# Kernel tuning notes

Measured on AMD Instinct MI355X. Metric: run time of the kernel, lower is better.

Reference implementation:

```python
import jax, jax.numpy as jnp
import numpy as np

N_NODES = 20000
N_EDGES = 160000
IN_DIM = 2048
HID = 512


def setup_inputs() -> dict:
    key = jax.random.key(0)
    ks = jax.random.split(key, 12)
    s1 = 1.0 / np.sqrt(IN_DIM)
    s2 = 1.0 / np.sqrt(HID)
    return {
        "x": jax.random.normal(ks[0], (N_NODES, IN_DIM), dtype=jnp.float32),
        "edge_index": jax.random.randint(ks[1], (2, N_EDGES), 0, N_NODES, dtype=jnp.int64),
        "W1": jax.random.uniform(ks[2], (IN_DIM, HID), jnp.float32, -s1, s1),
        "b1": jax.random.uniform(ks[3], (HID,), jnp.float32, -s1, s1),
        "W2": jax.random.uniform(ks[4], (HID, HID), jnp.float32, -s2, s2),
        "b2": jax.random.uniform(ks[5], (HID,), jnp.float32, -s2, s2),
        "Wg": jax.random.uniform(ks[6], (HID, HID), jnp.float32, -s2, s2),
        "bg": jax.random.uniform(ks[7], (HID,), jnp.float32, -s2, s2),
        "Wa": jax.random.uniform(ks[8], (HID, 1), jnp.float32, -s2, s2),
        "ba": jax.random.uniform(ks[9], (1,), jnp.float32, -s2, s2),
    }


def reference(x, edge_index, W1, b1, W2, b2, Wg, bg, Wa, ba):
    # GINConv (eps=0): h = MLP((1+eps)*x + sum_{j in N(i)} x_j)
    src, dst = edge_index[0], edge_index[1]
    agg = jax.ops.segment_sum(x[src], dst, num_segments=x.shape[0])  # [N, IN_DIM]
    h = x + agg
    h = jnp.maximum(h @ W1 + b1, 0.0) @ W2 + b2  # [N, HID]
    # Gated attention pooling scores
    A = jnp.tanh(h @ Wg + bg)                    # [N, HID]
    alpha = (A @ Wa + ba)[:, 0]                  # [N]
    att_scores = jax.nn.softmax(alpha, axis=0)   # softmax over all nodes
    return (h, att_scores)
```

## Files before the change

### kernel.cpp

```cpp
#include <hip/hip_runtime.h>

typedef __attribute__((ext_vector_type(8))) __bf16 bf16x8;
typedef __attribute__((ext_vector_type(4))) __bf16 bf16x4;
typedef __attribute__((ext_vector_type(4))) float f32x4;
typedef __attribute__((ext_vector_type(8))) unsigned short u16x8;

__device__ __forceinline__ bf16x8 cvt8(float4 a, float4 b) {
    bf16x8 o;
    o[0] = (__bf16)a.x; o[1] = (__bf16)a.y; o[2] = (__bf16)a.z; o[3] = (__bf16)a.w;
    o[4] = (__bf16)b.x; o[5] = (__bf16)b.y; o[6] = (__bf16)b.z; o[7] = (__bf16)b.w;
    return o;
}
__device__ __forceinline__ bf16x4 cvt4(f32x4 v) {
    bf16x4 o;
    o[0] = (__bf16)v[0]; o[1] = (__bf16)v[1]; o[2] = (__bf16)v[2]; o[3] = (__bf16)v[3];
    return o;
}

__device__ __forceinline__ unsigned swz(int row, int s) {
    return (unsigned)((row * 64 + s * 16) ^ ((row & 8) << 2));
}

#define GLDS(g, l) __builtin_amdgcn_global_load_lds(                        \
    (const __attribute__((address_space(1))) void*)(g),                     \
    (__attribute__((address_space(3))) void*)(l), 16, 0, 0)

__global__ __launch_bounds__(256) void convw_pre_kernel(const float* __restrict__ W,
                                                        char* __restrict__ out, int K) {
    int t = blockIdx.x * 256 + threadIdx.x;
    if (t >= K * 512) return;
    int k = t >> 9, n = t & 511;
    int cb = n >> 8, r = n & 255, tt = k >> 5, s = (k & 31) >> 3, e = k & 7;
    size_t off = ((size_t)cb * (K >> 5) + tt) * 16384 + swz(r, s) + e * 2;
    *(__bf16*)(out + off) = (__bf16)W[t];
}

__global__ __launch_bounds__(256) void count_kernel(const int* __restrict__ dst,
                                                    int* __restrict__ counts, int E) {
    int e = blockIdx.x * 256 + threadIdx.x;
    if (e < E) atomicAdd(&counts[dst[e]], 1);
}

__global__ __launch_bounds__(1024) void scan_kernel(const int* __restrict__ counts,
                                                    int* __restrict__ offs, int N) {
    __shared__ int wsum[16], wpre[16];
    const int CH = 20;
    int tid = threadIdx.x, lane = tid & 63, wv = tid >> 6;
    int base = tid * CH;
    int s = 0;
    for (int i = 0; i < CH; i++) { int idx = base + i; s += (idx < N) ? counts[idx] : 0; }
    int run = s;
#pragma unroll
    for (int o = 1; o < 64; o <<= 1) { int v = __shfl_up(run, o, 64); if (lane >= o) run += v; }
    if (lane == 63) wsum[wv] = run;
    __syncthreads();
    if (tid == 0) { int acc = 0; for (int w = 0; w < 16; w++) { wpre[w] = acc; acc += wsum[w]; } }
    __syncthreads();
    int pre = wpre[wv] + (run - s);
    for (int i = 0; i < CH; i++) {
        int idx = base + i;
        if (idx <= N) offs[idx] = pre;
        pre += (idx < N) ? counts[idx] : 0;
    }
}

__global__ __launch_bounds__(256) void bucket_kernel(const int* __restrict__ src,
                                                     const int* __restrict__ dst,
                                                     const int* __restrict__ offs,
                                                     int* __restrict__ cursor,
                                                     int* __restrict__ eids, int E) {
    int e = blockIdx.x * 256 + threadIdx.x;
    if (e >= E) return;
    int d = dst[e];
    int pos = atomicAdd(&cursor[d], 1);
    eids[offs[d] + pos] = src[e];
}

__global__ __launch_bounds__(256) void gather_h1_kernel(const float* __restrict__ y,
                                                        const int* __restrict__ offs,
                                                        const int* __restrict__ eids,
                                                        const float* __restrict__ b1,
                                                        __bf16* __restrict__ h1b,
                                                        int N) {
    int node = blockIdx.x * 2 + (threadIdx.x >> 7);
    if (node >= N) return;
    int c = (threadIdx.x & 127) << 2;
    float4 s = *(const float4*)(y + (size_t)node * 512 + c);
    int beg = offs[node], end = offs[node + 1];
    for (int k = beg; k < end; k++) {
        int sn = eids[k];
        const float4 v = *(const float4*)(y + (size_t)sn * 512 + c);
        s.x += v.x; s.y += v.y; s.z += v.z; s.w += v.w;
    }
    const float4 b = *(const float4*)(b1 + c);
    f32x4 r;
    r[0] = fmaxf(s.x + b.x, 0.f);
    r[1] = fmaxf(s.y + b.y, 0.f);
    r[2] = fmaxf(s.z + b.z, 0.f);
    r[3] = fmaxf(s.w + b.w, 0.f);
    *(bf16x4*)(h1b + (size_t)node * 512 + c) = cvt4(r);
}

template <int KDIM, int AMODE, int EPI>
__global__ __launch_bounds__(256) void gemm_sec(const void* __restrict__ Asrc,
                                                const char* __restrict__ Bpre,
                                                const float* __restrict__ bias,
                                                float* __restrict__ Cf,
                                                char* __restrict__ hbpre,
                                                const float* __restrict__ Wa,
                                                float* __restrict__ alphaOut,
                                                int M) {
    constexpr int NT = KDIM / 32;
    __shared__ char smem[40960];
    const int tid = threadIdx.x, lane = tid & 63, wv = tid >> 6;
    const int fr = lane & 15, sec = lane >> 4, hi4 = (lane >> 4) * 4;
    const long row0 = (long)blockIdx.x * 64;
    const int cb = blockIdx.y;
    const char* Bp = Bpre + (size_t)cb * NT * 16384;

    f32x4 acc[4][4];
#pragma unroll
    for (int m = 0; m < 4; m++)
#pragma unroll
        for (int n = 0; n < 4; n++)
#pragma unroll
            for (int r = 0; r < 4; r++) acc[m][n][r] = 0.f;

    const int as_ = tid & 3, ar_ = tid >> 2;
    const unsigned awz = swz(ar_, as_);
    long arow = row0 + ar_; if (arow > (long)M - 1) arow = M - 1;
    const float* ApF = (const float*)Asrc + arow * KDIM + as_ * 8;
    const char*  ApH = (const char*)Asrc + arow * (KDIM * 2) + as_ * 16;
    const char*  ApT = (const char*)Asrc + (size_t)blockIdx.x * 65536;

#define ASEC(b) (smem + (b) * 4096)
#define BSEC(b) (smem + 8192 + (b) * 16384)
#define STAGE_B(buf, t) do {                                              \
        const char* src_ = Bp + (size_t)(t) * 16384;                      \
        _Pragma("unroll") for (int c_ = 0; c_ < 4; c_++)                  \
            GLDS(src_ + tid * 16 + c_ * 4096, BSEC(buf) + tid * 16 + c_ * 4096); \
    } while (0)

    STAGE_B(0, 0);
    if constexpr (AMODE == 0) {
        float4 a0 = *(const float4*)(ApF), a1 = *(const float4*)(ApF + 4);
        *(bf16x8*)(ASEC(0) + awz) = cvt8(a0, a1);
    } else if constexpr (AMODE == 1) {
        u16x8 v = *(const u16x8*)(ApH);
        *(u16x8*)(ASEC(0) + awz) = v;
    } else {
        GLDS(ApT + tid * 16, ASEC(0) + tid * 16);
    }
    __syncthreads();

    for (int t = 0; t < NT; t++) {
        const int cur = t & 1, nxt = cur ^ 1;
        const bool more = (t + 1 < NT);
        float4 a0, a1; u16x8 av;
        if (more) {
            STAGE_B(nxt, t + 1);
            if constexpr (AMODE == 0) {
                a0 = *(const float4*)(ApF + (t + 1) * 32);
                a1 = *(const float4*)(ApF + (t + 1) * 32 + 4);
            } else if constexpr (AMODE == 1) {
                av = *(const u16x8*)(ApH + (t + 1) * 64);
            } else {
                GLDS(ApT + (size_t)(t + 1) * 4096 + tid * 16, ASEC(nxt) + tid * 16);
            }
        }
        bf16x8 wf[4], xf[4];
#pragma unroll
        for (int m = 0; m < 4; m++)
            wf[m] = *(const bf16x8*)(BSEC(cur) + swz(wv * 64 + m * 16 + fr, sec));
#pragma unroll
        for (int n = 0; n < 4; n++)
            xf[n] = *(const bf16x8*)(ASEC(cur) + swz(n * 16 + fr, sec));
#pragma unroll
        for (int m = 0; m < 4; m++)
#pragma unroll
            for (int n = 0; n < 4; n++)
                acc[m][n] = __builtin_amdgcn_mfma_f32_16x16x32_bf16(wf[m], xf[n], acc[m][n], 0, 0, 0);
        if (more) {
            if constexpr (AMODE == 0) {
                *(bf16x8*)(ASEC(nxt) + awz) = cvt8(a0, a1);
            } else if constexpr (AMODE == 1) {
                *(u16x8*)(ASEC(nxt) + awz) = av;
            }
        }
        __syncthreads();
    }

    if constexpr (EPI == 0) {
#pragma unroll
        for (int n = 0; n < 4; n++) {
            long node = row0 + n * 16 + fr;
            if (node < M) {
#pragma unroll
                for (int m = 0; m < 4; m++)
                    *(f32x4*)(Cf + node * 512 + cb * 256 + wv * 64 + m * 16 + hi4) = acc[m][n];
            }
        }
    } else if constexpr (EPI == 1) {
#pragma unroll
        for (int n = 0; n < 4; n++) {
            int nodeloc = n * 16 + fr;
            long node = row0 + nodeloc;
#pragma unroll
            for (int m = 0; m < 4; m++) {
                int hc = cb * 256 + wv * 64 + m * 16 + hi4;
                f32x4 bv = *(const f32x4*)(bias + hc);
                f32x4 v = acc[m][n] + bv;
                if (node < M) *(f32x4*)(Cf + node * 512 + hc) = v;
                int tt = hc >> 5, ss = (hc & 31) >> 3, e = hc & 7;
                *(bf16x4*)(hbpre + (size_t)blockIdx.x * 65536 + (size_t)tt * 4096 +
                           swz(nodeloc, ss) + e * 2) = cvt4(v);
            }
        }
    } else {
        float* aS = (float*)smem;
        if (tid < 64) aS[tid] = 0.f;
        __syncthreads();
#pragma unroll
        for (int n = 0; n < 4; n++) {
            float s = 0.f;
#pragma unroll
            for (int m = 0; m < 4; m++) {
                int gc = cb * 256 + wv * 64 + m * 16 + hi4;
                f32x4 bgv = *(const f32x4*)(bias + gc);
                f32x4 wav = *(const f32x4*)(Wa + gc);
#pragma unroll
                for (int r = 0; r < 4; r++)
                    s += tanhf(acc[m][n][r] + bgv[r]) * wav[r];
            }
            atomicAdd(&aS[n * 16 + fr], s);
        }
        __syncthreads();
        if (tid < 64) {
            long node = row0 + tid;
            if (node < M) atomicAdd(&alphaOut[node], aS[tid]);
        }
    }
#undef ASEC
#undef BSEC
#undef STAGE_B
}

__global__ __launch_bounds__(1024) void softmax_kernel(const float* __restrict__ alpha,
                                                       float* __restrict__ att, int N) {
    __shared__ float red[16];
    __shared__ float bc[2];
    int tid = threadIdx.x, lane = tid & 63, wv = tid >> 6;
    float m = -3.4e38f;
    for (int i = tid; i < N; i += 1024) m = fmaxf(m, alpha[i]);
#pragma unroll
    for (int o = 32; o > 0; o >>= 1) m = fmaxf(m, __shfl_xor(m, o, 64));
    if (lane == 0) red[wv] = m;
    __syncthreads();
    if (tid == 0) {
        float mm = red[0];
        for (int i = 1; i < 16; i++) mm = fmaxf(mm, red[i]);
        bc[0] = mm;
    }
    __syncthreads();
    float Mx = bc[0];
    float s = 0.f;
    for (int i = tid; i < N; i += 1024) s += expf(alpha[i] - Mx);
#pragma unroll
    for (int o = 32; o > 0; o >>= 1) s += __shfl_xor(s, o, 64);
    if (lane == 0) red[wv] = s;
    __syncthreads();
    if (tid == 0) {
        float ss = 0.f;
        for (int i = 0; i < 16; i++) ss += red[i];
        bc[1] = ss;
    }
    __syncthreads();
    float inv = 1.f / bc[1];
    for (int i = tid; i < N; i += 1024) att[i] = expf(alpha[i] - Mx) * inv;
}

extern "C" void kernel_launch(void* const* d_in, const int* in_sizes, int n_in,
                              void* d_out, int out_size, void* d_ws, size_t ws_size,
                              hipStream_t stream) {
    const float* x  = (const float*)d_in[0];
    const int*   ei = (const int*)d_in[1];
    const float* W1 = (const float*)d_in[2];
    const float* b1 = (const float*)d_in[3];
    const float* W2 = (const float*)d_in[4];
    const float* b2 = (const float*)d_in[5];
    const float* Wg = (const float*)d_in[6];
    const float* bg = (const float*)d_in[7];
    const float* Wa = (const float*)d_in[8];

    const int M = 20000, IN = 2048, H = 512, E = 160000;

    char* ws = (char*)d_ws;
    float* y      = (float*)ws;
    char*  W1p    = ws + 40960000;
    char*  W2p    = ws + 43057152;
    char*  Wgp    = ws + 43581440;
    __bf16* h1b   = (__bf16*)(ws + 44105728);
    char*  hbpre  = ws + 64585728;
    float* alpha  = (float*)(ws + 85098496);
    int*   counts = (int*)(ws + 85178496);
    int*   offs   = (int*)(ws + 85258496);
    int*   cursor = (int*)(ws + 85338504);
    int*   eids   = (int*)(ws + 85418504);

    float* hout = (float*)d_out;
    float* att  = hout + (size_t)M * H;

    convw_pre_kernel<<<4096, 256, 0, stream>>>(W1, W1p, IN);
    convw_pre_kernel<<<1024, 256, 0, stream>>>(W2, W2p, H);
    convw_pre_kernel<<<1024, 256, 0, stream>>>(Wg, Wgp, H);

    hipMemsetAsync(counts, 0, M * 4, stream);
    count_kernel<<<(E + 255) / 256, 256, 0, stream>>>(ei + E, counts, E);
    scan_kernel<<<1, 1024, 0, stream>>>(counts, offs, M);
    hipMemsetAsync(cursor, 0, M * 4, stream);
    bucket_kernel<<<(E + 255) / 256, 256, 0, stream>>>(ei, ei + E, offs, cursor, eids, E);

    gemm_sec<2048, 0, 0><<<dim3(313, 2), 256, 0, stream>>>(x, W1p, nullptr, y, nullptr, nullptr, nullptr, M);

    gather_h1_kernel<<<10000, 256, 0, stream>>>(y, offs, eids, b1, h1b, M);

    gemm_sec<512, 1, 1><<<dim3(313, 2), 256, 0, stream>>>(h1b, W2p, b2, hout, hbpre, nullptr, nullptr, M);

    hipMemsetAsync(alpha, 0, M * 4, stream);
    gemm_sec<512, 2, 2><<<dim3(313, 2), 256, 0, stream>>>(hbpre, Wgp, bg, nullptr, nullptr, Wa, alpha, M);

    softmax_kernel<<<1, 1024, 0, stream>>>(alpha, att, M);
}
```

Before: 281.3 us.

## Read GEMM weight fragments directly from global memory, drop pre-tiled h buffer

The GEMM kernel stops staging the B (weight) tiles in LDS with global_load_lds and instead loads MFMA weight fragments straight from the pre-swizzled global buffer, shrinking shared memory from 40KB to 16KB. The A tile now covers 64 K-elements per barrier, which halves the number of synchronisations. The second GEMM no longer writes a bf16 pre-tiled copy of h, and the gate GEMM re-reads fp32 h and converts it on the fly. This trades LDS traffic and barriers for more global/L2 weight reads per wave and an extra fp32 read of h, while allowing higher occupancy.

Result: no change. 279.9 us (-0.5%).

```diff
diff --git a/kernel.cpp b/kernel.cpp
--- a/kernel.cpp
+++ b/kernel.cpp
@@ -20,10 +20,6 @@
 __device__ __forceinline__ unsigned swz(int row, int s) {
     return (unsigned)((row * 64 + s * 16) ^ ((row & 8) << 2));
 }
-
-#define GLDS(g, l) __builtin_amdgcn_global_load_lds(                        \
-    (const __attribute__((address_space(1))) void*)(g),                     \
-    (__attribute__((address_space(3))) void*)(l), 16, 0, 0)
 
 __global__ __launch_bounds__(256) void convw_pre_kernel(const float* __restrict__ W,
                                                         char* __restrict__ out, int K) {
@@ -102,21 +98,20 @@
 }
 
 template <int KDIM, int AMODE, int EPI>
-__global__ __launch_bounds__(256) void gemm_sec(const void* __restrict__ Asrc,
-                                                const char* __restrict__ Bpre,
-                                                const float* __restrict__ bias,
-                                                float* __restrict__ Cf,
-                                                char* __restrict__ hbpre,
-                                                const float* __restrict__ Wa,
-                                                float* __restrict__ alphaOut,
-                                                int M) {
-    constexpr int NT = KDIM / 32;
-    __shared__ char smem[40960];
+__global__ __launch_bounds__(256) void gemm_nb(const void* __restrict__ Asrc,
+                                               const char* __restrict__ Bpre,
+                                               const float* __restrict__ bias,
+                                               float* __restrict__ Cf,
+                                               const float* __restrict__ Wa,
+                                               float* __restrict__ alphaOut,
+                                               int M) {
+    constexpr int NT2 = KDIM / 64;
+    __shared__ char smem[16384];
     const int tid = threadIdx.x, lane = tid & 63, wv = tid >> 6;
     const int fr = lane & 15, sec = lane >> 4, hi4 = (lane >> 4) * 4;
     const long row0 = (long)blockIdx.x * 64;
     const int cb = blockIdx.y;
-    const char* Bp = Bpre + (size_t)cb * NT * 16384;
+    const char* Bp = Bpre + (size_t)cb * (KDIM / 32) * 16384;
 
     f32x4 acc[4][4];
 #pragma unroll
@@ -126,68 +121,76 @@
 #pragma unroll
             for (int r = 0; r < 4; r++) acc[m][n][r] = 0.f;
 
-    const int as_ = tid & 3, ar_ = tid >> 2;
-    const unsigned awz = swz(ar_, as_);
+    const int ar_ = tid >> 2, ks = tid & 3;
+    const unsigned awz = swz(ar_, ks);
     long arow = row0 + ar_; if (arow > (long)M - 1) arow = M - 1;
-    const float* ApF = (const float*)Asrc + arow * KDIM + as_ * 8;
-    const char*  ApH = (const char*)Asrc + arow * (KDIM * 2) + as_ * 16;
-    const char*  ApT = (const char*)Asrc + (size_t)blockIdx.x * 65536;
-
-#define ASEC(b) (smem + (b) * 4096)
-#define BSEC(b) (smem + 8192 + (b) * 16384)
-#define STAGE_B(buf, t) do {                                              \
-        const char* src_ = Bp + (size_t)(t) * 16384;                      \
-        _Pragma("unroll") for (int c_ = 0; c_ < 4; c_++)                  \
-            GLDS(src_ + tid * 16 + c_ * 4096, BSEC(buf) + tid * 16 + c_ * 4096); \
-    } while (0)
-
-    STAGE_B(0, 0);
+    const float* ApF = (const float*)Asrc + arow * KDIM;
+    const char*  ApH = (const char*)Asrc + arow * (KDIM * 2);
+
+#define ASEC(b) (smem + (b) * 8192)
+
     if constexpr (AMODE == 0) {
-        float4 a0 = *(const float4*)(ApF), a1 = *(const float4*)(ApF + 4);
+        float4 a0 = *(const float4*)(ApF + ks * 8);
+        float4 a1 = *(const float4*)(ApF + ks * 8 + 4);
+        float4 a2 = *(const float4*)(ApF + 32 + ks * 8);
+        float4 a3 = *(const float4*)(ApF + 32 + ks * 8 + 4);
         *(bf16x8*)(ASEC(0) + awz) = cvt8(a0, a1);
-    } else if constexpr (AMODE == 1) {
-        u16x8 v = *(const u16x8*)(ApH);
-        *(u16x8*)(ASEC(0) + awz) = v;
+        *(bf16x8*)(ASEC(0) + 4096 + awz) = cvt8(a2, a3);
     } else {
-        GLDS(ApT + tid * 16, ASEC(0) + tid * 16);
-    }
-    __syncthreads();
-
-    for (int t = 0; t < NT; t++) {
-        const int cur = t & 1, nxt = cur ^ 1;
-        const bool more = (t + 1 < NT);
-        float4 a0, a1; u16x8 av;
-        if (more) {
-            STAGE_B(nxt, t + 1);
-            if constexpr (AMODE == 0) {
-                a0 = *(const float4*)(ApF + (t + 1) * 32);
-                a1 = *(const float4*)(ApF + (t + 1) * 32 + 4);
-            } else if constexpr (AMODE == 1) {
-                av = *(const u16x8*)(ApH + (t + 1) * 64);
-            } else {
-                GLDS(ApT + (size_t)(t + 1) * 4096 + tid * 16, ASEC(nxt) + tid * 16);
-            }
-        }
-        bf16x8 wf[4], xf[4];
-#pragma unroll
-        for (int m = 0; m < 4; m++)
-            wf[m] = *(const bf16x8*)(BSEC(cur) + swz(wv * 64 + m * 16 + fr, sec));
-#pragma unroll
-        for (int n = 0; n < 4; n++)
-            xf[n] = *(const bf16x8*)(ASEC(cur) + swz(n * 16 + fr, sec));
-#pragma unroll
-        for (int m = 0; m < 4; m++)
-#pragma unroll
-            for (int n = 0; n < 4; n++)
-                acc[m][n] = __builtin_amdgcn_mfma_f32_16x16x32_bf16(wf[m], xf[n], acc[m][n], 0, 0, 0);
+        u16x8 v0 = *(const u16x8*)(ApH + ks * 16);
+        u16x8 v1 = *(const u16x8*)(ApH + 64 + ks * 16);
+        *(u16x8*)(ASEC(0) + awz) = v0;
+        *(u16x8*)(ASEC(0) + 4096 + awz) = v1;
+    }
+    asm volatile("s_waitcnt lgkmcnt(0)" ::: "memory");
+    __builtin_amdgcn_s_barrier();
+
+    int cur = 0;
+    for (int tt = 0; tt < NT2; tt++) {
+        const bool more = (tt + 1 < NT2);
+        float4 a0, a1, a2, a3; u16x8 v0, v1;
         if (more) {
             if constexpr (AMODE == 0) {
+                const float* p = ApF + (tt + 1) * 64;
+                a0 = *(const float4*)(p + ks * 8);
+                a1 = *(const float4*)(p + ks * 8 + 4);
+                a2 = *(const float4*)(p + 32 + ks * 8);
+                a3 = *(const float4*)(p + 32 + ks * 8 + 4);
+            } else {
+                const char* p = ApH + (size_t)(tt + 1) * 128;
+                v0 = *(const u16x8*)(p + ks * 16);
+                v1 = *(const u16x8*)(p + 64 + ks * 16);
+            }
+        }
+#pragma unroll
+        for (int h = 0; h < 2; h++) {
+            const char* bt = Bp + (size_t)(tt * 2 + h) * 16384;
+            bf16x8 wf[4], xf[4];
+#pragma unroll
+            for (int m = 0; m < 4; m++)
+                wf[m] = *(const bf16x8*)(bt + swz(wv * 64 + m * 16 + fr, sec));
+#pragma unroll
+            for (int n = 0; n < 4; n++)
+                xf[n] = *(const bf16x8*)(ASEC(cur) + h * 4096 + swz(n * 16 + fr, sec));
+#pragma unroll
+            for (int m = 0; m < 4; m++)
+#pragma unroll
+                for (int n = 0; n < 4; n++)
+                    acc[m][n] = __builtin_amdgcn_mfma_f32_16x16x32_bf16(wf[m], xf[n], acc[m][n], 0, 0, 0);
+        }
+        if (more) {
+            const int nxt = cur ^ 1;
+            if constexpr (AMODE == 0) {
                 *(bf16x8*)(ASEC(nxt) + awz) = cvt8(a0, a1);
-            } else if constexpr (AMODE == 1) {
-                *(u16x8*)(ASEC(nxt) + awz) = av;
-            }
-        }
-        __syncthreads();
+                *(bf16x8*)(ASEC(nxt) + 4096 + awz) = cvt8(a2, a3);
+            } else {
+                *(u16x8*)(ASEC(nxt) + awz) = v0;
+                *(u16x8*)(ASEC(nxt) + 4096 + awz) = v1;
+            }
+            asm volatile("s_waitcnt lgkmcnt(0)" ::: "memory");
+            __builtin_amdgcn_s_barrier();
+            cur = nxt;
+        }
     }
 
     if constexpr (EPI == 0) {
@@ -203,20 +206,18 @@
     } else if constexpr (EPI == 1) {
 #pragma unroll
         for (int n = 0; n < 4; n++) {
-            int nodeloc = n * 16 + fr;
-            long node = row0 + nodeloc;
-#pragma unroll
-            for (int m = 0; m < 4; m++) {
-                int hc = cb * 256 + wv * 64 + m * 16 + hi4;
-                f32x4 bv = *(const f32x4*)(bias + hc);
-                f32x4 v = acc[m][n] + bv;
-                if (node < M) *(f32x4*)(Cf + node * 512 + hc) = v;
-                int tt = hc >> 5, ss = (hc & 31) >> 3, e = hc & 7;
-                *(bf16x4*)(hbpre + (size_t)blockIdx.x * 65536 + (size_t)tt * 4096 +
-                           swz(nodeloc, ss) + e * 2) = cvt4(v);
+            long node = row0 + n * 16 + fr;
+            if (node < M) {
+#pragma unroll
+                for (int m = 0; m < 4; m++) {
+                    int hc = cb * 256 + wv * 64 + m * 16 + hi4;
+                    f32x4 bv = *(const f32x4*)(bias + hc);
+                    *(f32x4*)(Cf + node * 512 + hc) = acc[m][n] + bv;
+                }
             }
         }
     } else {
+        __syncthreads();
         float* aS = (float*)smem;
         if (tid < 64) aS[tid] = 0.f;
         __syncthreads();
@@ -241,8 +242,6 @@
         }
     }
 #undef ASEC
-#undef BSEC
-#undef STAGE_B
 }
 
 __global__ __launch_bounds__(1024) void softmax_kernel(const float* __restrict__ alpha,
@@ -300,12 +299,11 @@
     char*  W2p    = ws + 43057152;
     char*  Wgp    = ws + 43581440;
     __bf16* h1b   = (__bf16*)(ws + 44105728);
-    char*  hbpre  = ws + 64585728;
-    float* alpha  = (float*)(ws + 85098496);
-    int*   counts = (int*)(ws + 85178496);
-    int*   offs   = (int*)(ws + 85258496);
-    int*   cursor = (int*)(ws + 85338504);
-    int*   eids   = (int*)(ws + 85418504);
+    float* alpha  = (float*)(ws + 64585728);
+    int*   counts = (int*)(ws + 64665728);
+    int*   offs   = (int*)(ws + 64745728);
+    int*   cursor = (int*)(ws + 64825732);
+    int*   eids   = (int*)(ws + 64905732);
 
     float* hout = (float*)d_out;
     float* att  = hout + (size_t)M * H;
@@ -320,14 +318,14 @@
     hipMemsetAsync(cursor, 0, M * 4, stream);
     bucket_kernel<<<(E + 255) / 256, 256, 0, stream>>>(ei, ei + E, offs, cursor, eids, E);
 
-    gemm_sec<2048, 0, 0><<<dim3(313, 2), 256, 0, stream>>>(x, W1p, nullptr, y, nullptr, nullptr, nullptr, M);
+    gemm_nb<2048, 0, 0><<<dim3(313, 2), 256, 0, stream>>>(x, W1p, nullptr, y, nullptr, nullptr, M);
 
     gather_h1_kernel<<<10000, 256, 0, stream>>>(y, offs, eids, b1, h1b, M);
 
-    gemm_sec<512, 1, 1><<<dim3(313, 2), 256, 0, stream>>>(h1b, W2p, b2, hout, hbpre, nullptr, nullptr, M);
+    gemm_nb<512, 1, 1><<<dim3(313, 2), 256, 0, stream>>>(h1b, W2p, b2, hout, nullptr, nullptr, M);
 
     hipMemsetAsync(alpha, 0, M * 4, stream);
-    gemm_sec<512, 2, 2><<<dim3(313, 2), 256, 0, stream>>>(hbpre, Wgp, bg, nullptr, nullptr, Wa, alpha, M);
+    gemm_nb<512, 0, 2><<<dim3(313, 2), 256, 0, stream>>>(hout, Wgp, bg, nullptr, Wa, alpha, M);
 
     softmax_kernel<<<1, 1024, 0, stream>>>(alpha, att, M);
 }
```
